# Kernel optimization log

Measured on AMD Instinct MI355X. Metric: run time of the kernel, lower is better.

The kernel has to match this reference:

```python
import jax, jax.numpy as jnp
import numpy as np

N, E, F, EF, D, G = 25000, 100000, 32, 8, 64, 1000


def setup_inputs() -> dict:
    key = jax.random.key(0)
    ks = jax.random.split(key, 32)
    p = lambda k, shape: (jax.random.normal(k, shape, jnp.float32) * 0.05)
    inp = {
        "x": jax.random.normal(ks[0], (N, F), jnp.float32),
        "edge_index": jax.random.randint(ks[1], (2, E), 0, N, jnp.int64 if jax.config.jax_enable_x64 else jnp.int32),
        "edge_attr": jax.random.uniform(ks[2], (E, EF), jnp.float32),
        "batch": jnp.sort(jax.random.randint(ks[3], (N,), 0, G, jnp.int32)),
        # lin0
        "W0": p(ks[4], (F, D)), "b0": p(ks[5], (D,)),
        # edge MLP: Linear(EF, D) -> ReLU -> Linear(D, D*D)
        "We1": p(ks[6], (EF, D)), "be1": p(ks[7], (D,)),
        "We2": p(ks[8], (D, D * D)), "be2": p(ks[9], (D * D,)),
        # NNConv root weight + bias
        "Wroot": p(ks[10], (D, D)), "bconv": p(ks[11], (D,)),
        # GRU (single layer): gate order r, z, n
        "Wi": p(ks[12], (3 * D, D)), "Wh": p(ks[13], (3 * D, D)),
        "bi": p(ks[14], (3 * D,)), "bh": p(ks[15], (3 * D,)),
        # heads
        "W11": p(ks[16], (D, D)), "b11": p(ks[17], (D,)),
        "W12": p(ks[18], (D, D)), "b12": p(ks[19], (D,)),
        "W13": p(ks[20], (D, 1)), "b13": p(ks[21], (1,)),
        "W21": p(ks[22], (D, D)), "b21": p(ks[23], (D,)),
        "W22": p(ks[24], (D, D)), "b22": p(ks[25], (D,)),
        "W23": p(ks[26], (D, 1)), "b23": p(ks[27], (1,)),
    }
    return inp


def reference(x, edge_index, edge_attr, batch,
              W0, b0, We1, be1, We2, be2, Wroot, bconv,
              Wi, Wh, bi, bh,
              W11, b11, W12, b12, W13, b13,
              W21, b21, W22, b22, W23, b23):
    src, dst = edge_index[0], edge_index[1]
    # lin0 + relu
    x1 = jax.nn.relu(x @ W0 + b0)                      # [N, D]
    h = x1                                              # GRU hidden init
    # NNConv: dynamic per-edge weight via edge MLP
    ew = (jax.nn.relu(edge_attr @ We1 + be1) @ We2 + be2).reshape(E, D, D)
    msg = jnp.einsum('ei,eio->eo', x1[src], ew)        # per-edge matmul
    agg = jax.ops.segment_sum(msg, dst, num_segments=N)
    x2 = jax.nn.relu(x1 @ Wroot + agg + bconv)         # [N, D]
    # GRU single step (torch gate order: r, z, n)
    gi = x2 @ Wi.T + bi
    gh = h @ Wh.T + bh
    r = jax.nn.sigmoid(gi[:, :D] + gh[:, :D])
    z = jax.nn.sigmoid(gi[:, D:2 * D] + gh[:, D:2 * D])
    n = jnp.tanh(gi[:, 2 * D:] + r * gh[:, 2 * D:])
    hn = (1.0 - z) * n + z * h                          # [N, D]
    # graph pooling (scatter_add over batch)
    pooled = jax.ops.segment_sum(hn, batch, num_segments=G)  # [G, D]
    # two MLP heads
    x_1 = jax.nn.relu(pooled @ W11 + b11)
    x_1 = jax.nn.relu(x_1 @ W12 + b12)
    x_1 = x_1 @ W13 + b13
    x_2 = jax.nn.relu(pooled @ W21 + b21)
    x_2 = jax.nn.relu(x_2 @ W22 + b22)
    x_2 = x_2 @ W23 + b23
    return jnp.concatenate([x_1, x_2], axis=1)          # [G, 2]
```

## Files before the change

### kernel.cpp

```cpp
#include <hip/hip_runtime.h>
#include <hip/hip_bf16.h>
#include <hip/hip_fp16.h>

#define NN 25000
#define NE 100000
#define FIN 32
#define DD 64
#define NG 1000

typedef unsigned short u16;
typedef __attribute__((ext_vector_type(8))) short short8;
typedef __attribute__((ext_vector_type(8))) _Float16 f16x8;
typedef __attribute__((ext_vector_type(4))) float f32x4;

__device__ __forceinline__ u16 f2h(float f) {
    __half h = __float2half(f);
    return __builtin_bit_cast(u16, h);
}
__device__ __forceinline__ float h2f(u16 u) {
    __half h = __builtin_bit_cast(__half, u);
    return __half2float(h);
}
__device__ __forceinline__ f16x8 s2h(short8 v) { return __builtin_bit_cast(f16x8, v); }
__device__ __forceinline__ short8 scale8(short8 v, __half2 t) {
    union { short8 s; __half2 h[4]; } u; u.s = v;
    u.h[0] = __hmul2(u.h[0], t);
    u.h[1] = __hmul2(u.h[1], t);
    u.h[2] = __hmul2(u.h[2], t);
    u.h[3] = __hmul2(u.h[3], t);
    return u.s;
}
__device__ __forceinline__ bool idx_is_i64(const int* e) {
    return (e[1] == 0) & (e[3] == 0) & (e[5] == 0) & (e[7] == 0) & (e[9] == 0);
}
__device__ __forceinline__ int ld_src(const int* e, int i, bool i64) {
    return i64 ? e[2 * i] : e[i];
}
__device__ __forceinline__ int ld_dst(const int* e, int i, bool i64) {
    return i64 ? e[2 * (NE + i)] : e[NE + i];
}

__global__ __launch_bounds__(256) void k_pre(const float* __restrict__ x,
                                             const float* __restrict__ W0,
                                             const float* __restrict__ b0,
                                             u16* __restrict__ x1b,
                                             const float* __restrict__ We2,
                                             const float* __restrict__ be2,
                                             float* __restrict__ agg,
                                             float* __restrict__ pooled,
                                             u16* __restrict__ Bt2,
                                             const float* __restrict__ Wi,
                                             const float* __restrict__ Wh,
                                             const float* __restrict__ Wroot,
                                             u16* __restrict__ Wib,
                                             u16* __restrict__ Whb,
                                             u16* __restrict__ Wrb) {
    __shared__ float sbuf[4096 + 512];
    int tid = threadIdx.x;
    if (blockIdx.x < 1563) {
        float* sW = sbuf;
        float* sx = sbuf + 4096;
        for (int i = tid; i < FIN * DD; i += 256) sW[i] = W0[i];
        int nbase = blockIdx.x * 16;
        for (int i = tid; i < 16 * FIN; i += 256) {
            int nl = i >> 5, f = i & 31;
            int n = nbase + nl;
            sx[i] = (n < NN) ? x[n * FIN + f] : 0.f;
        }
        __syncthreads();
        int lane = tid & 63, nl = tid >> 6;
        float bias = b0[lane];
        #pragma unroll
        for (int rr = 0; rr < 4; rr++) {
            int row = nl * 4 + rr;
            int n = nbase + row;
            if (n < NN) {
                float acc = bias;
                #pragma unroll
                for (int f = 0; f < FIN; f++) acc += sx[row * FIN + f] * sW[f * DD + lane];
                x1b[n * DD + lane] = f2h(fmaxf(acc, 0.f));
            }
        }
    } else if (blockIdx.x < 1628) {
        int kc = blockIdx.x - 1563;
        const float* src = (kc < 64) ? (We2 + kc * 4096) : be2;
        for (int i = tid; i < 4096; i += 256) sbuf[i] = src[i];
        __syncthreads();
        for (int m = tid; m < 4096; m += 256) {
            int f = m >> 9, ln = (m >> 3) & 63, j = m & 7;
            int s = f >> 2, c = f & 3;
            int o = c * 16 + (ln & 15);
            int rlow = s * 32 + (ln >> 4) * 8 + j;
            Bt2[kc * 4096 + m] = f2h(sbuf[rlow * 64 + o]);
        }
    } else {
        int tid0 = (blockIdx.x - 1628) * 256 + threadIdx.x;
        const int STR = 256 * 256;
        for (int i = tid0; i < NN * DD; i += STR) agg[i] = 0.f;
        for (int i = tid0; i < NG * DD; i += STR) pooled[i] = 0.f;
        for (int i = tid0; i < 12288; i += STR) {
            int fr = i >> 9, lane = (i >> 3) & 63, j = i & 7;
            int c = fr >> 1, kcx = fr & 1;
            int row = c * 16 + (lane & 15);
            int col = kcx * 32 + (lane >> 4) * 8 + j;
            Wib[i] = f2h(Wi[row * 64 + col]);
            Whb[i] = f2h(Wh[row * 64 + col]);
        }
        for (int i = tid0; i < 4096; i += STR) {
            int fr = i >> 9, lane = (i >> 3) & 63, j = i & 7;
            int c = fr >> 1, kcx = fr & 1;
            int row = c * 16 + (lane & 15);
            int col = kcx * 32 + (lane >> 4) * 8 + j;
            Wrb[i] = f2h(Wroot[col * 64 + row]);
        }
    }
}

__global__ __launch_bounds__(512, 4) void k_msg(const float* __restrict__ ea,
                                                const int* __restrict__ eidx,
                                                const float* __restrict__ We1,
                                                const float* __restrict__ be1,
                                                const u16* __restrict__ x1b,
                                                const u16* __restrict__ Bt2,
                                                float* __restrict__ agg) {
    __shared__ __align__(16) u16 sX[128 * 72];
    __shared__ __align__(16) float sT[65 * 128];
    __shared__ float sWe1[8 * 64];
    __shared__ float sbe1[64];
    __shared__ int sDst[128];
    const int tid = threadIdx.x;
    const int lane = tid & 63, wv = tid >> 6;
    const int ll = lane & 15, quad = lane >> 4;
    const int rh = wv >> 2, cq = wv & 3;
    const int e0 = blockIdx.x * 128;
    const bool i64 = idx_is_i64(eidx);

    if (tid < 512) sWe1[tid] = We1[tid];
    if (tid < 64) sbe1[tid] = be1[tid];
    if (tid < 128) {
        sDst[tid] = (e0 + tid < NE) ? ld_dst(eidx, e0 + tid, i64) : 0;
        sT[64 * 128 + tid] = 1.0f;
    }

    const int el4 = tid >> 2, seg = tid & 3;
    const int eg4 = e0 + el4;
    {
        if (eg4 < NE) {
            int sv = ld_src(eidx, eg4, i64);
            const u16* xr = x1b + sv * 64 + seg * 16;
            *(uint4*)&sX[el4 * 72 + seg * 16]     = *(const uint4*)(xr);
            *(uint4*)&sX[el4 * 72 + seg * 16 + 8] = *(const uint4*)(xr + 8);
        } else {
            uint4 z = make_uint4(0, 0, 0, 0);
            *(uint4*)&sX[el4 * 72 + seg * 16]     = z;
            *(uint4*)&sX[el4 * 72 + seg * 16 + 8] = z;
        }
    }
    float eav[8];
    if (eg4 < NE) {
        f32x4 v0 = *(const f32x4*)(ea + eg4 * 8);
        f32x4 v1 = *(const f32x4*)(ea + eg4 * 8 + 4);
        #pragma unroll
        for (int f = 0; f < 4; f++) { eav[f] = v0[f]; eav[4 + f] = v1[f]; }
    } else {
        #pragma unroll
        for (int f = 0; f < 8; f++) eav[f] = 0.f;
    }
    __syncthreads();

    {
        int eh = el4 & 63;
        const int tpos = (el4 >> 6) * 64 + (eh & 15) * 4 + (eh >> 4);
        int k0 = seg * 16;
        for (int kk = 0; kk < 16; kk++) {
            int k = k0 + kk;
            float acc = sbe1[k];
            #pragma unroll
            for (int f = 0; f < 8; f++) acc += eav[f] * sWe1[f * 64 + k];
            sT[k * 128 + tpos] = (eg4 < NE) ? fmaxf(acc, 0.f) : 0.f;
        }
    }
    __syncthreads();

    short8 xa[4][2];
    #pragma unroll
    for (int rt = 0; rt < 4; rt++)
        #pragma unroll
        for (int s = 0; s < 2; s++)
            xa[rt][s] = *(const short8*)&sX[(rh * 64 + rt * 16 + ll) * 72 + s * 32 + quad * 8];

    f32x4 acc[4];
    #pragma unroll
    for (int rt = 0; rt < 4; rt++) acc[rt] = (f32x4){0.f, 0.f, 0.f, 0.f};

    const u16* gB0 = Bt2 + (0 * 4 + cq) * 512 + lane * 8;
    const u16* gB1 = Bt2 + (1 * 4 + cq) * 512 + lane * 8;

    short8 c0 = *(const short8*)(gB0);
    short8 c1 = *(const short8*)(gB1);

    for (int kc = 0; kc < 65; kc++) {
        int kn = (kc < 64) ? kc + 1 : 64;
        short8 n0 = *(const short8*)(gB0 + kn * 4096);
        short8 n1 = *(const short8*)(gB1 + kn * 4096);
        f32x4 tq = *(const f32x4*)&sT[kc * 128 + rh * 64 + ll * 4];
        f16x8 b0 = s2h(c0), b1 = s2h(c1);
        #pragma unroll
        for (int rt = 0; rt < 4; rt++) {
            __half2 th = __float2half2_rn(tq[rt]);
            f16x8 a0 = s2h(scale8(xa[rt][0], th));
            f16x8 a1 = s2h(scale8(xa[rt][1], th));
            acc[rt] = __builtin_amdgcn_mfma_f32_16x16x32_f16(a0, b0, acc[rt], 0, 0, 0);
            acc[rt] = __builtin_amdgcn_mfma_f32_16x16x32_f16(a1, b1, acc[rt], 0, 0, 0);
        }
        c0 = n0; c1 = n1;
    }

    #pragma unroll
    for (int rt = 0; rt < 4; rt++) {
        #pragma unroll
        for (int r = 0; r < 4; r++) {
            int el = rh * 64 + rt * 16 + quad * 4 + r;
            int eg = e0 + el;
            if (eg < NE) {
                int d = sDst[el];
                atomicAdd(&agg[d * 64 + cq * 16 + ll], acc[rt][r]);
            }
        }
    }
}

__global__ __launch_bounds__(256) void k_gru(const u16* __restrict__ x1b,
                                             const float* __restrict__ agg,
                                             const u16* __restrict__ Wib,
                                             const u16* __restrict__ Whb,
                                             const u16* __restrict__ Wrb,
                                             const float* __restrict__ bconv,
                                             const float* __restrict__ bi,
                                             const float* __restrict__ bh,
                                             const int* __restrict__ batch,
                                             float* __restrict__ pooled) {
    __shared__ __align__(16) u16 sX2[64 * 72];
    __shared__ float hbuf[64 * 65];
    __shared__ int sBatch[64];
    const int tid = threadIdx.x;
    const int lane = tid & 63, wv = tid >> 6;
    const int ll = lane & 15, quad = lane >> 4;
    const int n0 = blockIdx.x * 64;

    if (tid < 64) {
        int n = n0 + tid;
        sBatch[tid] = (n < NN) ? batch[n] : -1;
    }

    short8 ha[2];
    {
        int n = n0 + wv * 16 + ll;
        #pragma unroll
        for (int kc = 0; kc < 2; kc++) {
            if (n < NN) ha[kc] = *(const short8*)(x1b + n * 64 + kc * 32 + quad * 8);
            else        ha[kc] = (short8){0,0,0,0,0,0,0,0};
        }
    }
    f32x4 acc1[4];
    #pragma unroll
    for (int c = 0; c < 4; c++) acc1[c] = (f32x4){0.f, 0.f, 0.f, 0.f};
    #pragma unroll
    for (int kc = 0; kc < 2; kc++) {
        #pragma unroll
        for (int c = 0; c < 4; c++) {
            short8 b = *(const short8*)&Wrb[(c * 2 + kc) * 512 + lane * 8];
            acc1[c] = __builtin_amdgcn_mfma_f32_16x16x32_f16(s2h(ha[kc]), s2h(b), acc1[c], 0, 0, 0);
        }
    }
    #pragma unroll
    for (int c = 0; c < 4; c++) {
        int col = c * 16 + ll;
        float bcv = bconv[col];
        #pragma unroll
        for (int r = 0; r < 4; r++) {
            int row = wv * 16 + quad * 4 + r;
            int n = n0 + row;
            float v = 0.f;
            if (n < NN) v = fmaxf(acc1[c][r] + agg[n * 64 + col] + bcv, 0.f);
            sX2[row * 72 + col] = f2h(v);
        }
    }
    __syncthreads();

    short8 xa[2];
    #pragma unroll
    for (int kc = 0; kc < 2; kc++)
        xa[kc] = *(const short8*)&sX2[(wv * 16 + ll) * 72 + kc * 32 + quad * 8];

    f32x4 agi[12], agh[12];
    #pragma unroll
    for (int c = 0; c < 12; c++) { agi[c] = (f32x4){0.f,0.f,0.f,0.f}; agh[c] = (f32x4){0.f,0.f,0.f,0.f}; }
    #pragma unroll
    for (int kc = 0; kc < 2; kc++) {
        #pragma unroll
        for (int c = 0; c < 12; c++) {
            short8 bi8 = *(const short8*)&Wib[(c * 2 + kc) * 512 + lane * 8];
            short8 bh8 = *(const short8*)&Whb[(c * 2 + kc) * 512 + lane * 8];
            agi[c] = __builtin_amdgcn_mfma_f32_16x16x32_f16(s2h(xa[kc]), s2h(bi8), agi[c], 0, 0, 0);
            agh[c] = __builtin_amdgcn_mfma_f32_16x16x32_f16(s2h(ha[kc]), s2h(bh8), agh[c], 0, 0, 0);
        }
    }

    float hnv[4][4];
    #pragma unroll
    for (int c0 = 0; c0 < 4; c0++) {
        int d = c0 * 16 + ll;
        float bir = bi[d],        bhr = bh[d];
        float biz = bi[64 + d],   bhz = bh[64 + d];
        float bin = bi[128 + d],  bhn = bh[128 + d];
        #pragma unroll
        for (int r = 0; r < 4; r++) {
            int row = wv * 16 + quad * 4 + r;
            int n = n0 + row;
            float gir = agi[c0][r] + bir,     ghr = agh[c0][r] + bhr;
            float giz = agi[c0 + 4][r] + biz, ghz = agh[c0 + 4][r] + bhz;
            float gin = agi[c0 + 8][r] + bin, ghn = agh[c0 + 8][r] + bhn;
            float rg = 1.f / (1.f + __expf(-(gir + ghr)));
            float zg = 1.f / (1.f + __expf(-(giz + ghz)));
            float ng = tanhf(gin + rg * ghn);
            float hv = (n < NN) ? h2f(x1b[n * 64 + d]) : 0.f;
            hnv[c0][r] = (n < NN) ? ((1.f - zg) * ng + zg * hv) : 0.f;
        }
    }
    __syncthreads();

    #pragma unroll
    for (int c0 = 0; c0 < 4; c0++) {
        int d = c0 * 16 + ll;
        #pragma unroll
        for (int r = 0; r < 4; r++) {
            int row = wv * 16 + quad * 4 + r;
            hbuf[row * 65 + d] = hnv[c0][r];
        }
    }
    __syncthreads();

    {
        int d = lane;
        float sum = 0.f;
        int pb = sBatch[wv * 16];
        #pragma unroll
        for (int rr = 0; rr < 16; rr++) {
            int row = wv * 16 + rr;
            int b = sBatch[row];
            float v = hbuf[row * 65 + d];
            if (b != pb) {
                if (pb >= 0) atomicAdd(&pooled[pb * 64 + d], sum);
                sum = v; pb = b;
            } else {
                sum += v;
            }
        }
        if (pb >= 0) atomicAdd(&pooled[pb * 64 + d], sum);
    }
}

__global__ __launch_bounds__(256) void k_heads(const float* __restrict__ pooled,
                                               const float* __restrict__ W11, const float* __restrict__ b11,
                                               const float* __restrict__ W12, const float* __restrict__ b12,
                                               const float* __restrict__ W13, const float* __restrict__ b13,
                                               const float* __restrict__ W21, const float* __restrict__ b21,
                                               const float* __restrict__ W22, const float* __restrict__ b22,
                                               const float* __restrict__ W23, const float* __restrict__ b23,
                                               float* __restrict__ out) {
    __shared__ float sV[4][64];
    __shared__ float sA[4][64];
    int tid = threadIdx.x, lane = tid & 63, wv = tid >> 6;
    int g = blockIdx.x * 4 + wv;
    if (g >= NG) return;
    float p = pooled[g * 64 + lane];
    sV[wv][lane] = p;
    float y[2];
    const float* W1s[2] = {W11, W21}; const float* b1s[2] = {b11, b21};
    const float* W2s[2] = {W12, W22}; const float* b2s[2] = {b12, b22};
    const float* W3s[2] = {W13, W23}; const float* b3s[2] = {b13, b23};
    #pragma unroll
    for (int hd = 0; hd < 2; hd++) {
        float a = b1s[hd][lane];
        #pragma unroll 8
        for (int i = 0; i < 64; i++) a += sV[wv][i] * W1s[hd][i * 64 + lane];
        a = fmaxf(a, 0.f);
        sA[wv][lane] = a;
        float a2 = b2s[hd][lane];
        #pragma unroll 8
        for (int i = 0; i < 64; i++) a2 += sA[wv][i] * W2s[hd][i * 64 + lane];
        a2 = fmaxf(a2, 0.f);
        float part = a2 * W3s[hd][lane];
        #pragma unroll
        for (int m = 32; m > 0; m >>= 1) part += __shfl_xor(part, m, 64);
        y[hd] = part + b3s[hd][0];
    }
    if (lane == 0) {
        out[g * 2 + 0] = y[0];
        out[g * 2 + 1] = y[1];
    }
}

extern "C" void kernel_launch(void* const* d_in, const int* in_sizes, int n_in,
                              void* d_out, int out_size, void* d_ws, size_t ws_size,
                              hipStream_t stream) {
    const float* x     = (const float*)d_in[0];
    const int* eidx    = (const int*)d_in[1];
    const float* ea    = (const float*)d_in[2];
    const int* batch   = (const int*)d_in[3];
    const float* W0    = (const float*)d_in[4];  const float* b0    = (const float*)d_in[5];
    const float* We1   = (const float*)d_in[6];  const float* be1   = (const float*)d_in[7];
    const float* We2   = (const float*)d_in[8];  const float* be2   = (const float*)d_in[9];
    const float* Wroot = (const float*)d_in[10]; const float* bconv = (const float*)d_in[11];
    const float* Wi    = (const float*)d_in[12]; const float* Wh    = (const float*)d_in[13];
    const float* bi    = (const float*)d_in[14]; const float* bh    = (const float*)d_in[15];
    const float* W11   = (const float*)d_in[16]; const float* b11   = (const float*)d_in[17];
    const float* W12   = (const float*)d_in[18]; const float* b12   = (const float*)d_in[19];
    const float* W13   = (const float*)d_in[20]; const float* b13   = (const float*)d_in[21];
    const float* W21   = (const float*)d_in[22]; const float* b21   = (const float*)d_in[23];
    const float* W22   = (const float*)d_in[24]; const float* b22   = (const float*)d_in[25];
    const float* W23   = (const float*)d_in[26]; const float* b23   = (const float*)d_in[27];
    float* out = (float*)d_out;

    char* ws = (char*)d_ws;
    float* agg    = (float*)(ws);
    u16*   x1b    = (u16*)(ws + 6400000);
    u16*   Bt2    = (u16*)(ws + 9600000);
    float* pooled = (float*)(ws + 10132480);
    u16*   Wib    = (u16*)(ws + 10388480);
    u16*   Whb    = (u16*)(ws + 10413056);
    u16*   Wrb    = (u16*)(ws + 10437632);

    hipLaunchKernelGGL(k_pre, dim3(1884), dim3(256), 0, stream,
                       x, W0, b0, x1b, We2, be2, agg, pooled, Bt2,
                       Wi, Wh, Wroot, Wib, Whb, Wrb);
    hipLaunchKernelGGL(k_msg, dim3(782), dim3(512), 0, stream, ea, eidx, We1, be1, x1b, Bt2, agg);
    hipLaunchKernelGGL(k_gru, dim3(391), dim3(256), 0, stream, x1b, agg,
                       Wib, Whb, Wrb, bconv, bi, bh, batch, pooled);
    hipLaunchKernelGGL(k_heads, dim3(250), dim3(256), 0, stream, pooled,
                       W11, b11, W12, b12, W13, b13, W21, b21, W22, b22, W23, b23, out);
}
```

Before: 227.0 us.

## Restructure message kernel: unscaled MFMA with post-scaling, 1024-thread blocks, fp16 hidden tile

The per-edge message kernel no longer scales the gathered x1 operand by the hidden activation before each MFMA. It runs the MFMA against a zero accumulator and multiplies the result by the hidden value in fp32, with the hidden tile stored as fp16 and prefetched one step ahead. Blocks grow to 1024 threads, so each wave handles two row tiles instead of four. The lin0 part of the prep kernel now processes 64 nodes per block instead of 16. This removes the packed-half scaling work and should improve accuracy, at the cost of extra fp32 FMAs, fewer registers per thread and more waves per block.

```diff
diff --git a/kernel.cpp b/kernel.cpp
--- a/kernel.cpp
+++ b/kernel.cpp
@@ -22,14 +22,6 @@
     return __half2float(h);
 }
 __device__ __forceinline__ f16x8 s2h(short8 v) { return __builtin_bit_cast(f16x8, v); }
-__device__ __forceinline__ short8 scale8(short8 v, __half2 t) {
-    union { short8 s; __half2 h[4]; } u; u.s = v;
-    u.h[0] = __hmul2(u.h[0], t);
-    u.h[1] = __hmul2(u.h[1], t);
-    u.h[2] = __hmul2(u.h[2], t);
-    u.h[3] = __hmul2(u.h[3], t);
-    return u.s;
-}
 __device__ __forceinline__ bool idx_is_i64(const int* e) {
     return (e[1] == 0) & (e[3] == 0) & (e[5] == 0) & (e[7] == 0) & (e[9] == 0);
 }
@@ -57,22 +49,22 @@
                                              u16* __restrict__ Wrb) {
     __shared__ float sbuf[4096 + 512];
     int tid = threadIdx.x;
-    if (blockIdx.x < 1563) {
+    if (blockIdx.x < 391) {
         float* sW = sbuf;
-        float* sx = sbuf + 4096;
+        float* sx = sbuf + 2048;
         for (int i = tid; i < FIN * DD; i += 256) sW[i] = W0[i];
-        int nbase = blockIdx.x * 16;
-        for (int i = tid; i < 16 * FIN; i += 256) {
+        int nbase = blockIdx.x * 64;
+        for (int i = tid; i < 64 * FIN; i += 256) {
             int nl = i >> 5, f = i & 31;
             int n = nbase + nl;
             sx[i] = (n < NN) ? x[n * FIN + f] : 0.f;
         }
         __syncthreads();
-        int lane = tid & 63, nl = tid >> 6;
+        int lane = tid & 63, nl4 = tid >> 6;
         float bias = b0[lane];
         #pragma unroll
-        for (int rr = 0; rr < 4; rr++) {
-            int row = nl * 4 + rr;
+        for (int rr = 0; rr < 16; rr++) {
+            int row = nl4 * 16 + rr;
             int n = nbase + row;
             if (n < NN) {
                 float acc = bias;
@@ -81,8 +73,8 @@
                 x1b[n * DD + lane] = f2h(fmaxf(acc, 0.f));
             }
         }
-    } else if (blockIdx.x < 1628) {
-        int kc = blockIdx.x - 1563;
+    } else if (blockIdx.x < 456) {
+        int kc = blockIdx.x - 391;
         const float* src = (kc < 64) ? (We2 + kc * 4096) : be2;
         for (int i = tid; i < 4096; i += 256) sbuf[i] = src[i];
         __syncthreads();
@@ -94,7 +86,7 @@
             Bt2[kc * 4096 + m] = f2h(sbuf[rlow * 64 + o]);
         }
     } else {
-        int tid0 = (blockIdx.x - 1628) * 256 + threadIdx.x;
+        int tid0 = (blockIdx.x - 456) * 256 + threadIdx.x;
         const int STR = 256 * 256;
         for (int i = tid0; i < NN * DD; i += STR) agg[i] = 0.f;
         for (int i = tid0; i < NG * DD; i += STR) pooled[i] = 0.f;
@@ -116,15 +108,15 @@
     }
 }
 
-__global__ __launch_bounds__(512, 4) void k_msg(const float* __restrict__ ea,
-                                                const int* __restrict__ eidx,
-                                                const float* __restrict__ We1,
-                                                const float* __restrict__ be1,
-                                                const u16* __restrict__ x1b,
-                                                const u16* __restrict__ Bt2,
-                                                float* __restrict__ agg) {
+__global__ __launch_bounds__(1024, 4) void k_msg(const float* __restrict__ ea,
+                                                 const int* __restrict__ eidx,
+                                                 const float* __restrict__ We1,
+                                                 const float* __restrict__ be1,
+                                                 const u16* __restrict__ x1b,
+                                                 const u16* __restrict__ Bt2,
+                                                 float* __restrict__ agg) {
     __shared__ __align__(16) u16 sX[128 * 72];
-    __shared__ __align__(16) float sT[65 * 128];
+    __shared__ __align__(16) u16 sTh[65 * 128 + 64];
     __shared__ float sWe1[8 * 64];
     __shared__ float sbe1[64];
     __shared__ int sDst[128];
@@ -139,27 +131,23 @@
     if (tid < 64) sbe1[tid] = be1[tid];
     if (tid < 128) {
         sDst[tid] = (e0 + tid < NE) ? ld_dst(eidx, e0 + tid, i64) : 0;
-        sT[64 * 128 + tid] = 1.0f;
-    }
-
-    const int el4 = tid >> 2, seg = tid & 3;
-    const int eg4 = e0 + el4;
+        sTh[64 * 128 + tid] = 0x3C00;
+    }
+
+    const int el8 = tid >> 3, seg8 = tid & 7;
+    const int eg8 = e0 + el8;
     {
-        if (eg4 < NE) {
-            int sv = ld_src(eidx, eg4, i64);
-            const u16* xr = x1b + sv * 64 + seg * 16;
-            *(uint4*)&sX[el4 * 72 + seg * 16]     = *(const uint4*)(xr);
-            *(uint4*)&sX[el4 * 72 + seg * 16 + 8] = *(const uint4*)(xr + 8);
+        if (eg8 < NE) {
+            int sv = ld_src(eidx, eg8, i64);
+            *(uint4*)&sX[el8 * 72 + seg8 * 8] = *(const uint4*)(x1b + sv * 64 + seg8 * 8);
         } else {
-            uint4 z = make_uint4(0, 0, 0, 0);
-            *(uint4*)&sX[el4 * 72 + seg * 16]     = z;
-            *(uint4*)&sX[el4 * 72 + seg * 16 + 8] = z;
+            *(uint4*)&sX[el8 * 72 + seg8 * 8] = make_uint4(0, 0, 0, 0);
         }
     }
     float eav[8];
-    if (eg4 < NE) {
-        f32x4 v0 = *(const f32x4*)(ea + eg4 * 8);
-        f32x4 v1 = *(const f32x4*)(ea + eg4 * 8 + 4);
+    if (eg8 < NE) {
+        f32x4 v0 = *(const f32x4*)(ea + eg8 * 8);
+        f32x4 v1 = *(const f32x4*)(ea + eg8 * 8 + 4);
         #pragma unroll
         for (int f = 0; f < 4; f++) { eav[f] = v0[f]; eav[4 + f] = v1[f]; }
     } else {
@@ -169,62 +157,78 @@
     __syncthreads();
 
     {
-        int eh = el4 & 63;
-        const int tpos = (el4 >> 6) * 64 + (eh & 15) * 4 + (eh >> 4);
-        int k0 = seg * 16;
-        for (int kk = 0; kk < 16; kk++) {
+        int k0 = seg8 * 8;
+        for (int kk = 0; kk < 8; kk++) {
             int k = k0 + kk;
             float acc = sbe1[k];
             #pragma unroll
             for (int f = 0; f < 8; f++) acc += eav[f] * sWe1[f * 64 + k];
-            sT[k * 128 + tpos] = (eg4 < NE) ? fmaxf(acc, 0.f) : 0.f;
+            sTh[k * 128 + el8] = f2h((eg8 < NE) ? fmaxf(acc, 0.f) : 0.f);
         }
     }
     __syncthreads();
 
-    short8 xa[4][2];
-    #pragma unroll
-    for (int rt = 0; rt < 4; rt++)
+    short8 xa[2][2];
+    #pragma unroll
+    for (int rt = 0; rt < 2; rt++)
         #pragma unroll
         for (int s = 0; s < 2; s++)
-            xa[rt][s] = *(const short8*)&sX[(rh * 64 + rt * 16 + ll) * 72 + s * 32 + quad * 8];
-
-    f32x4 acc[4];
-    #pragma unroll
-    for (int rt = 0; rt < 4; rt++) acc[rt] = (f32x4){0.f, 0.f, 0.f, 0.f};
+            xa[rt][s] = *(const short8*)&sX[(rh * 32 + rt * 16 + ll) * 72 + s * 32 + quad * 8];
+
+    f32x4 msg[2];
+    #pragma unroll
+    for (int rt = 0; rt < 2; rt++) msg[rt] = (f32x4){0.f, 0.f, 0.f, 0.f};
 
     const u16* gB0 = Bt2 + (0 * 4 + cq) * 512 + lane * 8;
     const u16* gB1 = Bt2 + (1 * 4 + cq) * 512 + lane * 8;
+    const f32x4 zero = (f32x4){0.f, 0.f, 0.f, 0.f};
+    const int tkoff = rh * 32 + quad * 4;
+
+    #define LDR(dst, kcv, rtv) dst = *(const uint2*)&sTh[(kcv) * 128 + tkoff + (rtv) * 16];
+    #define CVT(t, raw)                                                      \
+        {                                                                    \
+            __half2 _a = __builtin_bit_cast(__half2, (raw).x);               \
+            __half2 _b = __builtin_bit_cast(__half2, (raw).y);               \
+            float2 _fa = __half22float2(_a);                                 \
+            float2 _fb = __half22float2(_b);                                 \
+            t = (f32x4){_fa.x, _fa.y, _fb.x, _fb.y};                         \
+        }
 
     short8 c0 = *(const short8*)(gB0);
     short8 c1 = *(const short8*)(gB1);
+    uint2 tkA[2], tkB[2];
+    #pragma unroll
+    for (int rt = 0; rt < 2; rt++) LDR(tkA[rt], 0, rt);
 
     for (int kc = 0; kc < 65; kc++) {
         int kn = (kc < 64) ? kc + 1 : 64;
         short8 n0 = *(const short8*)(gB0 + kn * 4096);
         short8 n1 = *(const short8*)(gB1 + kn * 4096);
-        f32x4 tq = *(const f32x4*)&sT[kc * 128 + rh * 64 + ll * 4];
-        f16x8 b0 = s2h(c0), b1 = s2h(c1);
-        #pragma unroll
-        for (int rt = 0; rt < 4; rt++) {
-            __half2 th = __float2half2_rn(tq[rt]);
-            f16x8 a0 = s2h(scale8(xa[rt][0], th));
-            f16x8 a1 = s2h(scale8(xa[rt][1], th));
-            acc[rt] = __builtin_amdgcn_mfma_f32_16x16x32_f16(a0, b0, acc[rt], 0, 0, 0);
-            acc[rt] = __builtin_amdgcn_mfma_f32_16x16x32_f16(a1, b1, acc[rt], 0, 0, 0);
+        #pragma unroll
+        for (int rt = 0; rt < 2; rt++) LDR(tkB[rt], kn, rt);
+        #pragma unroll
+        for (int rt = 0; rt < 2; rt++) {
+            f32x4 q0 = __builtin_amdgcn_mfma_f32_16x16x32_f16(s2h(xa[rt][0]), s2h(c0), zero, 0, 0, 0);
+            f32x4 q1 = __builtin_amdgcn_mfma_f32_16x16x32_f16(s2h(xa[rt][1]), s2h(c1), zero, 0, 0, 0);
+            f32x4 t; CVT(t, tkA[rt]);
+            msg[rt] += t * q0;
+            msg[rt] += t * q1;
         }
         c0 = n0; c1 = n1;
-    }
-
-    #pragma unroll
-    for (int rt = 0; rt < 4; rt++) {
+        tkA[0] = tkB[0]; tkA[1] = tkB[1];
+    }
+    #undef LDR
+    #undef CVT
+
+    #pragma unroll
+    for (int rt = 0; rt < 2; rt++) {
         #pragma unroll
         for (int r = 0; r < 4; r++) {
-            int el = rh * 64 + rt * 16 + quad * 4 + r;
+            int el = rh * 32 + rt * 16 + quad * 4 + r;
             int eg = e0 + el;
             if (eg < NE) {
                 int d = sDst[el];
-                atomicAdd(&agg[d * 64 + cq * 16 + ll], acc[rt][r]);
+                atomicAdd(&agg[d * 64 + cq * 16 + ll], msg[rt][r]);
             }
         }
     }
@@ -432,10 +436,10 @@
     u16*   Whb    = (u16*)(ws + 10413056);
     u16*   Wrb    = (u16*)(ws + 10437632);
 
-    hipLaunchKernelGGL(k_pre, dim3(1884), dim3(256), 0, stream,
+    hipLaunchKernelGGL(k_pre, dim3(712), dim3(256), 0, stream,
                        x, W0, b0, x1b, We2, be2, agg, pooled, Bt2,
                        Wi, Wh, Wroot, Wib, Whb, Wrb);
-    hipLaunchKernelGGL(k_msg, dim3(782), dim3(512), 0, stream, ea, eidx, We1, be1, x1b, Bt2, agg);
+    hipLaunchKernelGGL(k_msg, dim3(782), dim3(1024), 0, stream, ea, eidx, We1, be1, x1b, Bt2, agg);
     hipLaunchKernelGGL(k_gru, dim3(391), dim3(256), 0, stream, x1b, agg,
                        Wib, Whb, Wrb, bconv, bi, bh, batch, pooled);
     hipLaunchKernelGGL(k_heads, dim3(250), dim3(256), 0, stream, pooled,
```

Measured after the change: 238.7 us. 5.1% more time.
